# Optimization experiments

Hardware: AMD Instinct MI355X
Metric: run time of the kernel (lower is better)

The kernel has to match this reference:

```python
import jax, jax.numpy as jnp
import numpy as np

B, L, K, D = 1, 4096, 24, 512


def setup_inputs() -> dict:
    key = jax.random.key(0)
    k1, k2, k3, k4 = jax.random.split(key, 4)
    u = jax.random.normal(k1, (B, L, D), dtype=jnp.float32)
    # spectral filter bank (learned parameter initialized from Hankel eigenvectors in the
    # original; random init is equivalent for a correctness baseline), scaled ~O(1/sqrt(L))
    filters = jax.random.normal(k2, (L, K), dtype=jnp.float32) * (1.0 / np.sqrt(L))
    M_phi_plus = jax.random.normal(k3, (K, D, D), dtype=jnp.float32) * (1.0 / np.sqrt(K * D))
    M_phi_minus = jax.random.normal(k4, (K, D, D), dtype=jnp.float32) * (1.0 / np.sqrt(K * D))
    return {"u": u, "filters": filters, "M_phi_plus": M_phi_plus, "M_phi_minus": M_phi_minus}


def _causal_conv(u, phi):
    # Causal linear convolution of every input channel with every spectral filter via FFT.
    # u: [B, L, D], phi: [L, K] -> [B, L, K, D]
    L_ = u.shape[1]
    n = 2 * L_  # zero-pad so circular FFT conv == linear causal conv
    Uf = jnp.fft.rfft(u, n=n, axis=1)                    # [B, F, D]
    Pf = jnp.fft.rfft(phi, n=n, axis=0)                  # [F, K]
    prod = Uf[:, :, None, :] * Pf[None, :, :, None]      # [B, F, K, D]
    return jnp.fft.irfft(prod, n=n, axis=1)[:, :L_]      # [B, L, K, D]


def reference(u, filters, M_phi_plus, M_phi_minus):
    L_ = u.shape[1]
    # sgn[t] = (-1)^t ; U_minus[b,l,k,d] = sum_s u[b,s,d] * phi[l-s,k] * (-1)^(l-s),
    # which equals convolving with the alternating-sign filter phi[t]*(-1)^t
    # (the original implements this as sgn-pre/post-multiplication around FlashFFTConv).
    sgn = jnp.where(jnp.arange(L_) % 2 == 0, 1.0, -1.0).astype(u.dtype)
    U_plus = _causal_conv(u, filters)                      # [B, L, K, D]
    U_minus = _causal_conv(u, filters * sgn[:, None])      # [B, L, K, D]
    y = (jnp.einsum('blkd,kdo->blo', U_plus, M_phi_plus)
         + jnp.einsum('blkd,kdo->blo', U_minus, M_phi_minus))
    return y
```

## Files before the change

kernel.cpp:

```cpp
#include <hip/hip_runtime.h>
#include <hip/hip_bf16.h>
#include <cstdint>
#include <cstddef>

using bf16 = __hip_bfloat16;

typedef __attribute__((ext_vector_type(4))) float f32x4;
typedef __attribute__((ext_vector_type(8))) short s16x8;

#define LSEQ 4096
#define DDIM 512
#define KFLT 24
#define NFFT 8192
#define MR 8192

__device__ __forceinline__ void gld16(const bf16* g, bf16* l) {
  __builtin_amdgcn_global_load_lds((const __attribute__((address_space(1))) void*)g,
                                   (__attribute__((address_space(3))) void*)l, 16, 0, 0);
}

#define MEMFENCE asm volatile("" ::: "memory")
#define BAR() do { MEMFENCE; __builtin_amdgcn_s_barrier(); MEMFENCE; } while (0)

__device__ __forceinline__ float fsin_rev(float rev) {
  float s; asm("v_sin_f32 %0, %1" : "=v"(s) : "v"(rev)); return s;
}
__device__ __forceinline__ float fcos_rev(float rev) {
  float c; asm("v_cos_f32 %0, %1" : "=v"(c) : "v"(rev)); return c;
}

__device__ __forceinline__ void stage_half(const bf16* g, int ldk, bf16* ldsbase,
                                           int wave, int lane) {
  const int r8 = lane >> 3;
  const int sc = ((lane & 7) ^ r8) * 8;
  #pragma unroll
  for (int q = 0; q < 2; ++q) {
    const int c = wave * 2 + q;
    gld16(g + (size_t)(c * 8 + r8) * ldk + sc, ldsbase + c * 512);
  }
}

__device__ __forceinline__ s16x8 ldfrag(const bf16* buf, int row, int kk, int l4) {
  return *(const s16x8*)(buf + row * 64 + (((kk * 4 + l4) ^ (row & 7)) * 8));
}

__global__ __launch_bounds__(256) void transpose_cast(
    const float* __restrict__ in, bf16* __restrict__ out, int R, int C) {
  __shared__ float tile[32][33];
  const size_t bo = (size_t)blockIdx.z * R * C;
  const float* inb = in + bo;
  bf16* outb = out + bo;
  int c0 = blockIdx.x * 32, r0 = blockIdx.y * 32;
  int tx = threadIdx.x & 31, ty = threadIdx.x >> 5;
  #pragma unroll
  for (int i = 0; i < 32; i += 8)
    tile[ty + i][tx] = inb[(size_t)(r0 + ty + i) * C + (c0 + tx)];
  __syncthreads();
  #pragma unroll
  for (int i = 0; i < 32; i += 8)
    outb[(size_t)(c0 + ty + i) * R + (r0 + tx)] = __float2bfloat16(tile[tx][ty + i]);
}

__global__ __launch_bounds__(256) void add2_cast(
    const bf16* __restrict__ P, bf16* __restrict__ out) {
  size_t i = ((size_t)blockIdx.x * 256 + threadIdx.x) * 8;
  const size_t MN = (size_t)MR * DDIM;
  s16x8 a = *(const s16x8*)(P + i);
  s16x8 b = *(const s16x8*)(P + i + MN);
  bf16 o[8];
  #pragma unroll
  for (int e = 0; e < 8; ++e) {
    float fa = __uint_as_float((unsigned)(unsigned short)a[e] << 16);
    float fb = __uint_as_float((unsigned)(unsigned short)b[e] << 16);
    o[e] = __float2bfloat16(fa + fb);
  }
  *(s16x8*)(out + i) = *(const s16x8*)o;
}

__global__ __launch_bounds__(256) void tr_reduce4(
    const float* __restrict__ S, bf16* __restrict__ out) {
  __shared__ float tile[32][33];
  int c0 = blockIdx.x * 32, r0 = blockIdx.y * 32;
  int tx = threadIdx.x & 31, ty = threadIdx.x >> 5;
  const int nt = c0 >> 8;
  const int scl = (c0 & 255) + tx;
  const size_t SB = (size_t)MR * 256;
  #pragma unroll
  for (int i = 0; i < 32; i += 8) {
    size_t ro = (size_t)(r0 + ty + i) * 256 + scl;
    tile[ty + i][tx] = S[(0 * 2 + nt) * SB + ro] + S[(1 * 2 + nt) * SB + ro] +
                       S[(2 * 2 + nt) * SB + ro] + S[(3 * 2 + nt) * SB + ro];
  }
  __syncthreads();
  #pragma unroll
  for (int i = 0; i < 32; i += 8)
    out[(size_t)(c0 + ty + i) * MR + (r0 + tx)] = __float2bfloat16(tile[tx][ty + i]);
}

__global__ __launch_bounds__(256) void reduce4y(
    const float* __restrict__ P, const float* __restrict__ vnyq,
    float* __restrict__ y) {
  size_t i = ((size_t)blockIdx.x * 256 + threadIdx.x) * 4;
  const size_t MN = (size_t)LSEQ * DDIM;
  int l = (int)(i >> 9), o = (int)(i & 511);
  f32x4 a = *(const f32x4*)(P + i);
  f32x4 b = *(const f32x4*)(P + i + MN);
  f32x4 c = *(const f32x4*)(P + i + 2 * MN);
  f32x4 d = *(const f32x4*)(P + i + 3 * MN);
  f32x4 v = *(const f32x4*)(vnyq + o);
  float sg = (l & 1) ? -(1.f / NFFT) : (1.f / NFFT);
  f32x4 r = a + b + c + d;
  r[0] += sg * v[0]; r[1] += sg * v[1]; r[2] += sg * v[2]; r[3] += sg * v[3];
  *(f32x4*)(y + i) = r;
}

__global__ __launch_bounds__(256) void compute_pf(
    const float* __restrict__ phi, float* __restrict__ Pf) {
  int f0 = blockIdx.x * 2;
  int tid = threadIdx.x;
  int lane = tid & 63, wave = tid >> 6;
  float pre[2][KFLT], pim[2][KFLT];
  #pragma unroll
  for (int ff = 0; ff < 2; ++ff)
    #pragma unroll
    for (int k = 0; k < KFLT; ++k) { pre[ff][k] = 0.f; pim[ff][k] = 0.f; }
  for (int cch = 0; cch < LSEQ / 256; ++cch) {
    int t = cch * 256 + tid;
    const float4* pv = (const float4*)(phi + (size_t)t * KFLT);
    float4 v0 = pv[0], v1 = pv[1], v2 = pv[2], v3 = pv[3], v4 = pv[4], v5 = pv[5];
    float pr[KFLT] = {v0.x, v0.y, v0.z, v0.w, v1.x, v1.y, v1.z, v1.w,
                      v2.x, v2.y, v2.z, v2.w, v3.x, v3.y, v3.z, v3.w,
                      v4.x, v4.y, v4.z, v4.w, v5.x, v5.y, v5.z, v5.w};
    #pragma unroll
    for (int ff = 0; ff < 2; ++ff) {
      int m = ((f0 + ff) * t) & (NFFT - 1);
      float rev = (float)m * (1.f / NFFT);
      float s = fsin_rev(rev), c = fcos_rev(rev);
      #pragma unroll
      for (int k = 0; k < KFLT; ++k) {
        pre[ff][k] += pr[k] * c;
        pim[ff][k] -= pr[k] * s;
      }
    }
  }
  __shared__ float red[4][2][2 * KFLT];
  #pragma unroll
  for (int ff = 0; ff < 2; ++ff)
    #pragma unroll
    for (int k = 0; k < KFLT; ++k) {
      float r = pre[ff][k], i2 = pim[ff][k];
      #pragma unroll
      for (int off = 32; off > 0; off >>= 1) {
        r += __shfl_down(r, off, 64);
        i2 += __shfl_down(i2, off, 64);
      }
      if (lane == 0) { red[wave][ff][2 * k] = r; red[wave][ff][2 * k + 1] = i2; }
    }
  __syncthreads();
  if (tid < 96) {
    int ff = tid / 48, q = tid % 48;
    int f = f0 + ff;
    if (f <= NFFT / 2)
      Pf[(size_t)f * 48 + q] =
          red[0][ff][q] + red[1][ff][q] + red[2][ff][q] + red[3][ff][q];
  }
}

__global__ __launch_bounds__(256) void build_pw(
    const float* __restrict__ Pf, float* __restrict__ Pw, float* __restrict__ wnyq) {
  int idx = blockIdx.x * 256 + threadIdx.x;
  int j = idx >> 12, f = idx & 4095;
  float re, im;
  if (j < KFLT) {
    re = Pf[(size_t)f * 48 + j * 2];
    im = Pf[(size_t)f * 48 + j * 2 + 1];
  } else {
    int k = j - KFLT, g = NFFT / 2 - f;
    re = Pf[(size_t)g * 48 + k * 2];
    im = -Pf[(size_t)g * 48 + k * 2 + 1];
  }
  Pw[(size_t)idx * 2] = re;
  Pw[(size_t)idx * 2 + 1] = im;
  if (idx < 48)
    wnyq[idx] = (idx < KFLT) ? Pf[(size_t)(NFFT / 2) * 48 + idx * 2]
                             : Pf[(idx - KFLT) * 2];
}

__global__ __launch_bounds__(256) void nyq_u(
    const float* __restrict__ u, float* __restrict__ Unyq) {
  int d = blockIdx.x * 256 + threadIdx.x;
  int t0 = blockIdx.y * 64;
  float acc = 0.f;
  for (int t = t0; t < t0 + 64; t += 2)
    acc += u[(size_t)t * DDIM + d] - u[(size_t)(t + 1) * DDIM + d];
  atomicAdd(&Unyq[d], acc);
}

__global__ __launch_bounds__(256) void vnyq_k(
    const bf16* __restrict__ Mt, const float* __restrict__ Unyq,
    const float* __restrict__ wnyq, float* __restrict__ vnyq) {
  __shared__ float us[DDIM];
  int j = blockIdx.x, tid = threadIdx.x;
  us[tid] = Unyq[tid];
  us[tid + 256] = Unyq[tid + 256];
  __syncthreads();
  float w = wnyq[j];
  int o = blockIdx.y * 128 + (tid >> 1);
  int dh = (tid & 1) * 256;
  const bf16* row = Mt + ((size_t)j * DDIM + o) * DDIM + dh;
  float acc = 0.f;
  for (int d0 = 0; d0 < 256; d0 += 8) {
    s16x8 v = *(const s16x8*)(row + d0);
    #pragma unroll
    for (int e = 0; e < 8; ++e)
      acc += us[dh + d0 + e] * __uint_as_float((unsigned)(unsigned short)v[e] << 16);
  }
  acc += __shfl_xor(acc, 1, 64);
  if ((tid & 1) == 0) atomicAdd(&vnyq[o], w * acc);
}

template <int STORE>
__global__ __launch_bounds__(512, 2) void gemmG(
    const bf16* __restrict__ Bt, int ldk,
    bf16* __restrict__ Obf, float* __restrict__ Of) {
  __shared__ bf16 sA[3 * 128 * 64];
  __shared__ bf16 sB[3 * 256 * 64];

  const int lin = blockIdx.x;
  const int wid = (lin & 7) * 32 + (lin >> 3);

  int mt, nt, kt0, nkt, ks;
  if constexpr (STORE == 0) {
    ks = wid >> 7; int rem = wid & 127; mt = rem >> 1; nt = rem & 1;
    kt0 = ks * 32; nkt = 32;
  } else {
    ks = wid >> 6; int rem = wid & 63; mt = rem >> 1; nt = rem & 1;
    kt0 = ks * 32; nkt = 32;
  }

  const int tid = threadIdx.x, lane = tid & 63, wave = tid >> 6;
  const int l15 = lane & 15, l4 = lane >> 4;
  const int wr = wave >> 2, wc = wave & 3;
  const int r8 = lane >> 3, c8 = lane & 7;
  const int mtile = mt * 128, ntile = nt * 256;
  const bf16* Bb = Bt + (size_t)ntile * ldk;

  f32x4 acc[4][4];
  #pragma unroll
  for (int m = 0; m < 4; ++m)
    #pragma unroll
    for (int n = 0; n < 4; ++n) acc[m][n] = f32x4{0.f, 0.f, 0.f, 0.f};

  auto genA = [&](int t, int buf) {
    const int kbase = (kt0 + t) * 64 + ((c8 ^ r8) * 8);
    #pragma unroll
    for (int q = 0; q < 2; ++q) {
      const int c = wave * 2 + q;
      const int row = mtile + c * 8 + r8;
      bf16 o[8];
      if constexpr (STORE == 0) {
        const int f = row >> 1;
        const bool odd = row & 1;
        #pragma unroll
        for (int e = 0; e < 8; ++e) {
          int m = (f * (kbase + e)) & (NFFT - 1);
          float rev = (float)m * (1.f / NFFT);
          o[e] = __float2bfloat16(odd ? -fsin_rev(rev) : fcos_rev(rev));
        }
      } else {
        #pragma unroll
        for (int e = 0; e < 8; ++e) {
          int r = kbase + e;
          int f = r >> 1;
          int m = (f * row) & (NFFT - 1);
          float rev = (float)m * (1.f / NFFT);
          float sc2 = ((f == 0) ? 1.f : 2.f) * (1.f / NFFT);
          o[e] = __float2bfloat16((r & 1) ? -sc2 * fsin_rev(rev)
                                          : sc2 * fcos_rev(rev));
        }
      }
      *(s16x8*)(sA + buf * (128 * 64) + (c * 8 + r8) * 64 + c8 * 8) =
          *(const s16x8*)o;
    }
  };
  auto stageB = [&](int t, int buf) {
    const size_t ko = (size_t)(kt0 + t) * 64;
    stage_half(Bb + ko, ldk, sB + buf * (256 * 64), wave, lane);
    stage_half(Bb + (size_t)128 * ldk + ko, ldk, sB + buf * (256 * 64) + 128 * 64,
               wave, lane);
  };

  genA(0, 0);
  genA(1, 1);
  stageB(0, 0);
  stageB(1, 1);
  asm volatile("s_waitcnt vmcnt(4)" ::: "memory");
  asm volatile("s_waitcnt lgkmcnt(0)" ::: "memory");
  BAR();

  for (int t = 0; t < nkt; ++t) {
    const int buf = t % 3;
    const bf16* bA = sA + buf * (128 * 64);
    const bf16* bB = sB + buf * (256 * 64);
    const bool i2 = (t + 2 < nkt);

    s16x8 afr[4][2], bfr[4][2];
    #pragma unroll
    for (int n = 0; n < 4; ++n)
      #pragma unroll
      for (int kk = 0; kk < 2; ++kk)
        bfr[n][kk] = ldfrag(bB, wc * 64 + n * 16 + l15, kk, l4);
    #pragma unroll
    for (int m = 0; m < 4; ++m)
      #pragma unroll
      for (int kk = 0; kk < 2; ++kk)
        afr[m][kk] = ldfrag(bA, wr * 64 + m * 16 + l15, kk, l4);

    if (i2) {
      genA(t + 2, (t + 2) % 3);
      stageB(t + 2, (t + 2) % 3);
    }

    __builtin_amdgcn_s_setprio(1);
    #pragma unroll
    for (int m = 0; m < 4; ++m)
      #pragma unroll
      for (int n = 0; n < 4; ++n)
        #pragma unroll
        for (int kk = 0; kk < 2; ++kk)
          acc[m][n] = __builtin_amdgcn_mfma_f32_16x16x32_bf16(
              afr[m][kk], bfr[n][kk], acc[m][n], 0, 0, 0);
    __builtin_amdgcn_s_setprio(0);

    if (i2) { asm volatile("s_waitcnt vmcnt(4)" ::: "memory"); }
    else    { asm volatile("s_waitcnt vmcnt(0)" ::: "memory"); }
    asm volatile("s_waitcnt lgkmcnt(0)" ::: "memory");
    BAR();
  }

  #pragma unroll
  for (int m = 0; m < 4; ++m)
    #pragma unroll
    for (int n = 0; n < 4; ++n)
      #pragma unroll
      for (int e = 0; e < 4; ++e) {
        int row = mtile + wr * 64 + m * 16 + l4 * 4 + e;
        int col = ntile + wc * 64 + n * 16 + l15;
        if constexpr (STORE == 0)
          Obf[(size_t)ks * MR * DDIM + (size_t)row * DDIM + col] =
              __float2bfloat16(acc[m][n][e]);
        else
          Of[(size_t)ks * LSEQ * DDIM + (size_t)row * DDIM + col] = acc[m][n][e];
      }
}

__global__ __launch_bounds__(512, 2) void gemmW(
    const bf16* __restrict__ Auf, const bf16* __restrict__ Mt,
    const float* __restrict__ Pw, float* __restrict__ Slots) {
  __shared__ bf16 sB[3 * 256 * 64];
  __shared__ bf16 sA[256 * 64];
  __shared__ float2 sW[12 * 128];

  const int lin = blockIdx.x;
  const int q = lin & 7;
  const int pos = lin >> 3;
  const int jg = q >> 1, mhalf = q & 1;
  const int nt = pos >> 4;
  const int mt = mhalf * 16 + (pos & 15);

  const int tid = threadIdx.x, lane = tid & 63, wave = tid >> 6;
  const int l15 = lane & 15, l4 = lane >> 4;
  const int wr = wave >> 1, wc = wave & 1;

  float* dst = Slots + (size_t)(jg * 2 + nt) * ((size_t)MR * 256);

  f32x4 acc[4][8];
  #pragma unroll
  for (int m = 0; m < 4; ++m)
    #pragma unroll
    for (int n = 0; n < 8; ++n) acc[m][n] = f32x4{0.f, 0.f, 0.f, 0.f};

  auto stageB_ = [&](int s) {
    const int j = jg * 12 + (s % 12), kt = s / 12;
    const bf16* bb = Mt + (size_t)j * (DDIM * DDIM) + (size_t)(nt * 256) * DDIM + kt * 64;
    bf16* db = sB + (s % 3) * (256 * 64);
    stage_half(bb, DDIM, db, wave, lane);
    stage_half(bb + (size_t)128 * DDIM, DDIM, db + 128 * 64, wave, lane);
  };
  auto stageA_ = [&](int kt) {
    const bf16* ab = Auf + (size_t)(mt * 256) * DDIM + kt * 64;
    stage_half(ab, DDIM, sA, wave, lane);
    stage_half(ab + (size_t)128 * DDIM, DDIM, sA + 128 * 64, wave, lane);
  };

  #pragma unroll
  for (int t = 0; t < 3; ++t) {
    int idx = tid * 3 + t;
    int jj2 = idx >> 7, fo = idx & 127;
    sW[idx] = *(const float2*)(Pw +
        (((size_t)(jg * 12 + jj2)) * 4096 + (size_t)mt * 128 + fo) * 2);
  }
  stageB_(0);
  stageB_(1);
  stageA_(0);
  asm volatile("s_waitcnt vmcnt(0) lgkmcnt(0)" ::: "memory");
  BAR();

  int4 selfA[4][2];

  for (int s = 0; s < 96; ++s) {
    const int jj = s % 12, kt = s / 12;
    const bf16* bB = sB + (s % 3) * (256 * 64);

    if (s) {
      if (s == 95) { asm volatile("s_waitcnt vmcnt(0)" ::: "memory"); }
      else         { asm volatile("s_waitcnt vmcnt(4)" ::: "memory"); }
      BAR();
    }
    if (s + 2 < 96) stageB_(s + 2);
    if (jj == 6 && kt < 7) stageA_(kt + 1);

    if (jj == 0) {
      #pragma unroll
      for (int m = 0; m < 4; ++m)
        #pragma unroll
        for (int kk = 0; kk < 2; ++kk) {
          s16x8 v = ldfrag(sA, wr * 64 + m * 16 + l15, kk, l4);
          selfA[m][kk] = *(const int4*)&v;
        }
    }

    float wx[4], swy[4];
    #pragma unroll
    for (int m = 0; m < 4; ++m) {
      int fr = (wr * 64 + m * 16 + l15) >> 1;
      float2 w = sW[jj * 128 + fr];
      wx[m] = w.x;
      swy[m] = (l15 & 1) ? w.y : -w.y;
    }

    #pragma unroll
    for (int kk = 0; kk < 2; ++kk) {
      s16x8 bfr[8];
      #pragma unroll
      for (int n = 0; n < 8; ++n)
        bfr[n] = ldfrag(bB, wc * 128 + n * 16 + l15, kk, l4);
      #pragma unroll
      for (int m = 0; m < 4; ++m) {
        const int4 sv = selfA[m][kk];
        int4 pv;
        pv.x = __builtin_amdgcn_mov_dpp(sv.x, 0xB1, 0xF, 0xF, true);
        pv.y = __builtin_amdgcn_mov_dpp(sv.y, 0xB1, 0xF, 0xF, true);
        pv.z = __builtin_amdgcn_mov_dpp(sv.z, 0xB1, 0xF, 0xF, true);
        pv.w = __builtin_amdgcn_mov_dpp(sv.w, 0xB1, 0xF, 0xF, true);
        const int sp[4] = {sv.x, sv.y, sv.z, sv.w};
        const int pp[4] = {pv.x, pv.y, pv.z, pv.w};
        bf16 ob[8];
        #pragma unroll
        for (int t2 = 0; t2 < 4; ++t2) {
          float fsl = __uint_as_float((unsigned)sp[t2] << 16);
          float fsh = __uint_as_float((unsigned)sp[t2] & 0xffff0000u);
          float fpl = __uint_as_float((unsigned)pp[t2] << 16);
          float fph = __uint_as_float((unsigned)pp[t2] & 0xffff0000u);
          ob[2 * t2]     = __float2bfloat16(wx[m] * fsl + swy[m] * fpl);
          ob[2 * t2 + 1] = __float2bfloat16(wx[m] * fsh + swy[m] * fph);
        }
        const s16x8 afr = *(const s16x8*)ob;
        __builtin_amdgcn_s_setprio(1);
        #pragma unroll
        for (int n = 0; n < 8; ++n)
          acc[m][n] = __builtin_amdgcn_mfma_f32_16x16x32_bf16(
              afr, bfr[n], acc[m][n], 0, 0, 0);
        __builtin_amdgcn_s_setprio(0);
      }
    }
  }

  #pragma unroll
  for (int m = 0; m < 4; ++m)
    #pragma unroll
    for (int n = 0; n < 8; ++n)
      #pragma unroll
      for (int e = 0; e < 4; ++e) {
        int row = mt * 256 + wr * 64 + m * 16 + l4 * 4 + e;
        int col = wc * 128 + n * 16 + l15;
        dst[(size_t)row * 256 + col] = acc[m][n][e];
      }
}

#define WS_W     0ULL
#define WS_AUF   67108864ULL
#define WS_UT    75497472ULL
#define WS_MT    79691776ULL
#define WS_PF    104857600ULL
#define WS_PW    105644288ULL
#define WS_WNYQ  107217152ULL
#define WS_UNYQ  107217408ULL
#define WS_VNYQ  107219456ULL
#define WS_YBT   107221504ULL
#define WS_G1P   115610112ULL
#define WS_TOTAL 132387328ULL

extern "C" void kernel_launch(void* const* d_in, const int* in_sizes, int n_in,
                              void* d_out, int out_size, void* d_ws, size_t ws_size,
                              hipStream_t stream) {
  const float* u   = (const float*)d_in[0];
  const float* phi = (const float*)d_in[1];
  const float* Mp  = (const float*)d_in[2];
  const float* Mm  = (const float*)d_in[3];
  float* y = (float*)d_out;

  if (ws_size < WS_TOTAL) return;

  char* ws = (char*)d_ws;
  float* Slots= (float*)(ws + WS_W);
  bf16*  Auf  = (bf16*)(ws + WS_AUF);
  bf16*  uT   = (bf16*)(ws + WS_UT);
  bf16*  Mt   = (bf16*)(ws + WS_MT);
  float* Pf   = (float*)(ws + WS_PF);
  float* Pw   = (float*)(ws + WS_PW);
  float* wny  = (float*)(ws + WS_WNYQ);
  float* Uny  = (float*)(ws + WS_UNYQ);
  float* vny  = (float*)(ws + WS_VNYQ);
  bf16*  Ybt  = (bf16*)(ws + WS_YBT);
  bf16*  G1P  = (bf16*)(ws + WS_G1P);
  float* G3P  = (float*)(ws + WS_AUF);

  transpose_cast<<<dim3(16, 128, 1), 256, 0, stream>>>(u, uT, LSEQ, DDIM);
  transpose_cast<<<dim3(16, 16, 24), 256, 0, stream>>>(Mp, Mt, DDIM, DDIM);
  transpose_cast<<<dim3(16, 16, 24), 256, 0, stream>>>(Mm, Mt + (size_t)24 * DDIM * DDIM,
                                                       DDIM, DDIM);
  compute_pf<<<dim3(2049), 256, 0, stream>>>(phi, Pf);
  build_pw<<<dim3(48 * 4096 / 256), 256, 0, stream>>>(Pf, Pw, wny);
  hipMemsetAsync(Uny, 0, DDIM * sizeof(float), stream);
  nyq_u<<<dim3(2, 64), 256, 0, stream>>>(u, Uny);

  gemmG<0><<<256, 512, 0, stream>>>(uT, LSEQ, G1P, nullptr);
  add2_cast<<<dim3(MR * DDIM / 2048), 256, 0, stream>>>(G1P, Auf);

  gemmW<<<256, 512, 0, stream>>>(Auf, Mt, Pw, Slots);

  tr_reduce4<<<dim3(16, 256), 256, 0, stream>>>(Slots, Ybt);
  hipMemsetAsync(vny, 0, DDIM * sizeof(float), stream);
  vnyq_k<<<dim3(48, 4), 256, 0, stream>>>(Mt, Uny, wny, vny);

  gemmG<1><<<256, 512, 0, stream>>>(Ybt, MR, nullptr, G3P);
  reduce4y<<<dim3(LSEQ * DDIM / 1024), 256, 0, stream>>>(G3P, vny, y);
}
```

Baseline: 506.5 us.

## Double gemmW wavefronts per block, halving per-wave M tile

Raises gemmW from 512 to 1024 threads per block (16 waves), so each wave computes a 32x128 sub-tile instead of 64x128. Accumulator and A-fragment registers halve, LDS staging is spread across twice as many waves, and B fragments are loaded in two halves to save registers. This aims at more latency hiding through extra waves per CU. In exchange, B-fragment LDS reads per MFMA go up and the rotation/scaling VALU work is split more finely across waves. The launch_bounds of (1024, 4) asks for a very tight register budget, which may force spills.

New measurement: 484.3 us. -4.4%, faster.

```diff
diff --git a/kernel.cpp b/kernel.cpp
--- a/kernel.cpp
+++ b/kernel.cpp
@@ -38,6 +38,13 @@
     const int c = wave * 2 + q;
     gld16(g + (size_t)(c * 8 + r8) * ldk + sc, ldsbase + c * 512);
   }
+}
+
+__device__ __forceinline__ void stage16(const bf16* g, int ldk, bf16* ldsbase,
+                                        int wave, int lane) {
+  const int r8 = lane >> 3;
+  const int sc = ((lane & 7) ^ r8) * 8;
+  gld16(g + (size_t)(wave * 8 + r8) * ldk + sc, ldsbase + wave * 512);
 }
 
 __device__ __forceinline__ s16x8 ldfrag(const bf16* buf, int row, int kk, int l4) {
@@ -354,7 +361,7 @@
       }
 }
 
-__global__ __launch_bounds__(512, 2) void gemmW(
+__global__ __launch_bounds__(1024, 4) void gemmW(
     const bf16* __restrict__ Auf, const bf16* __restrict__ Mt,
     const float* __restrict__ Pw, float* __restrict__ Slots) {
   __shared__ bf16 sB[3 * 256 * 64];
@@ -374,9 +381,9 @@
 
   float* dst = Slots + (size_t)(jg * 2 + nt) * ((size_t)MR * 256);
 
-  f32x4 acc[4][8];
-  #pragma unroll
-  for (int m = 0; m < 4; ++m)
+  f32x4 acc[2][8];
+  #pragma unroll
+  for (int m = 0; m < 2; ++m)
     #pragma unroll
     for (int n = 0; n < 8; ++n) acc[m][n] = f32x4{0.f, 0.f, 0.f, 0.f};
 
@@ -384,18 +391,16 @@
     const int j = jg * 12 + (s % 12), kt = s / 12;
     const bf16* bb = Mt + (size_t)j * (DDIM * DDIM) + (size_t)(nt * 256) * DDIM + kt * 64;
     bf16* db = sB + (s % 3) * (256 * 64);
-    stage_half(bb, DDIM, db, wave, lane);
-    stage_half(bb + (size_t)128 * DDIM, DDIM, db + 128 * 64, wave, lane);
+    stage16(bb, DDIM, db, wave, lane);
+    stage16(bb + (size_t)128 * DDIM, DDIM, db + 128 * 64, wave, lane);
   };
   auto stageA_ = [&](int kt) {
     const bf16* ab = Auf + (size_t)(mt * 256) * DDIM + kt * 64;
-    stage_half(ab, DDIM, sA, wave, lane);
-    stage_half(ab + (size_t)128 * DDIM, DDIM, sA + 128 * 64, wave, lane);
+    stage16(ab, DDIM, sA, wave, lane);
+    stage16(ab + (size_t)128 * DDIM, DDIM, sA + 128 * 64, wave, lane);
   };
 
-  #pragma unroll
-  for (int t = 0; t < 3; ++t) {
-    int idx = tid * 3 + t;
+  for (int idx = tid; idx < 1536; idx += 1024) {
     int jj2 = idx >> 7, fo = idx & 127;
     sW[idx] = *(const float2*)(Pw +
         (((size_t)(jg * 12 + jj2)) * 4096 + (size_t)mt * 128 + fo) * 2);
@@ -406,7 +411,7 @@
   asm volatile("s_waitcnt vmcnt(0) lgkmcnt(0)" ::: "memory");
   BAR();
 
-  int4 selfA[4][2];
+  int4 selfA[2][2];
 
   for (int s = 0; s < 96; ++s) {
     const int jj = s % 12, kt = s / 12;
@@ -414,7 +419,7 @@
 
     if (s) {
       if (s == 95) { asm volatile("s_waitcnt vmcnt(0)" ::: "memory"); }
-      else         { asm volatile("s_waitcnt vmcnt(4)" ::: "memory"); }
+      else         { asm volatile("s_waitcnt vmcnt(2)" ::: "memory"); }
       BAR();
     }
     if (s + 2 < 96) stageB_(s + 2);
@@ -422,18 +427,18 @@
 
     if (jj == 0) {
       #pragma unroll
-      for (int m = 0; m < 4; ++m)
+      for (int m = 0; m < 2; ++m)
         #pragma unroll
         for (int kk = 0; kk < 2; ++kk) {
-          s16x8 v = ldfrag(sA, wr * 64 + m * 16 + l15, kk, l4);
+          s16x8 v = ldfrag(sA, wr * 32 + m * 16 + l15, kk, l4);
           selfA[m][kk] = *(const int4*)&v;
         }
     }
 
-    float wx[4], swy[4];
-    #pragma unroll
-    for (int m = 0; m < 4; ++m) {
-      int fr = (wr * 64 + m * 16 + l15) >> 1;
+    float wx[2], swy[2];
+    #pragma unroll
+    for (int m = 0; m < 2; ++m) {
+      int fr = (wr * 32 + m * 16 + l15) >> 1;
       float2 w = sW[jj * 128 + fr];
       wx[m] = w.x;
       swy[m] = (l15 & 1) ? w.y : -w.y;
@@ -441,12 +446,9 @@
 
     #pragma unroll
     for (int kk = 0; kk < 2; ++kk) {
-      s16x8 bfr[8];
-      #pragma unroll
-      for (int n = 0; n < 8; ++n)
-        bfr[n] = ldfrag(bB, wc * 128 + n * 16 + l15, kk, l4);
-      #pragma unroll
-      for (int m = 0; m < 4; ++m) {
+      s16x8 afr[2];
+      #pragma unroll
+      for (int m = 0; m < 2; ++m) {
         const int4 sv = selfA[m][kk];
         int4 pv;
         pv.x = __builtin_amdgcn_mov_dpp(sv.x, 0xB1, 0xF, 0xF, true);
@@ -465,24 +467,33 @@
           ob[2 * t2]     = __float2bfloat16(wx[m] * fsl + swy[m] * fpl);
           ob[2 * t2 + 1] = __float2bfloat16(wx[m] * fsh + swy[m] * fph);
         }
-        const s16x8 afr = *(const s16x8*)ob;
+        afr[m] = *(const s16x8*)ob;
+      }
+      #pragma unroll
+      for (int nh = 0; nh < 2; ++nh) {
+        s16x8 bfr[4];
+        #pragma unroll
+        for (int n = 0; n < 4; ++n)
+          bfr[n] = ldfrag(bB, wc * 128 + (nh * 4 + n) * 16 + l15, kk, l4);
         __builtin_amdgcn_s_setprio(1);
         #pragma unroll
-        for (int n = 0; n < 8; ++n)
-          acc[m][n] = __builtin_amdgcn_mfma_f32_16x16x32_bf16(
-              afr, bfr[n], acc[m][n], 0, 0, 0);
+        for (int m = 0; m < 2; ++m)
+          #pragma unroll
+          for (int n = 0; n < 4; ++n)
+            acc[m][nh * 4 + n] = __builtin_amdgcn_mfma_f32_16x16x32_bf16(
+                afr[m], bfr[n], acc[m][nh * 4 + n], 0, 0, 0);
         __builtin_amdgcn_s_setprio(0);
       }
     }
   }
 
   #pragma unroll
-  for (int m = 0; m < 4; ++m)
+  for (int m = 0; m < 2; ++m)
     #pragma unroll
     for (int n = 0; n < 8; ++n)
       #pragma unroll
       for (int e = 0; e < 4; ++e) {
-        int row = mt * 256 + wr * 64 + m * 16 + l4 * 4 + e;
+        int row = mt * 256 + wr * 32 + m * 16 + l4 * 4 + e;
         int col = wc * 128 + n * 16 + l15;
         dst[(size_t)row * 256 + col] = acc[m][n][e];
       }
@@ -538,7 +549,7 @@
   gemmG<0><<<256, 512, 0, stream>>>(uT, LSEQ, G1P, nullptr);
   add2_cast<<<dim3(MR * DDIM / 2048), 256, 0, stream>>>(G1P, Auf);
 
-  gemmW<<<256, 512, 0, stream>>>(Auf, Mt, Pw, Slots);
+  gemmW<<<256, 1024, 0, stream>>>(Auf, Mt, Pw, Slots);
 
   tr_reduce4<<<dim3(16, 256), 256, 0, stream>>>(Slots, Ybt);
   hipMemsetAsync(vny, 0, DDIM * sizeof(float), stream);
```
